# Optimization experiments

Hardware: AMD Instinct MI355X
Metric: run time of the kernel (lower is better)

## Reference

```python
import jax, jax.numpy as jnp
import numpy as np

K = 20
EPS = 1e-5   # BatchNorm eps (eval mode: running_mean=0, running_var=1)
SLOPE = 0.2


def knn_idx(x, k):
    # x: [B,F,N] -> idx [B,N,k]; top-k of negative squared distance (includes self)
    xx = jnp.sum(x * x, axis=1)                       # [B,N]
    inner = jnp.einsum('bfn,bfm->bnm', x, x)          # [B,N,N]
    neg_d = 2.0 * inner - xx[:, :, None] - xx[:, None, :]
    _, idx = jax.lax.top_k(neg_d, k)
    return idx


def gather_neighbors(x_nt, idx):
    # x_nt [B,N,F], idx [B,N,k] -> [B,N,k,F]
    return jax.vmap(lambda xt, ix: xt[ix])(x_nt, idx)


def group_layer(x_bfn, idx):
    # GroupLayer: [B,F,N] -> [B,2F,N,k] = cat(neigh - center, neigh)
    x_nt = jnp.transpose(x_bfn, (0, 2, 1))
    neigh = gather_neighbors(x_nt, idx)
    feat = jnp.concatenate([neigh - x_nt[:, :, None, :], neigh], axis=-1)
    return jnp.transpose(feat, (0, 3, 1, 2))


def eigen_graph(pts_bfn, k):
    # pts_bfn [B,3,N] -> feature [B,15,N], idx_EU [B,N,k], idx_EI [B,N,k]
    B, _, N = pts_bfn.shape
    idx_eu = knn_idx(pts_bfn, k)
    pts_nt = jnp.transpose(pts_bfn, (0, 2, 1))        # [B,N,3]
    neigh = gather_neighbors(pts_nt, idx_eu)          # [B,N,k,3]
    diff = neigh - pts_nt[:, :, None, :]
    cov = jnp.einsum('bnki,bnkj->bnij', diff, diff)   # [B,N,3,3] symmetric PSD
    eigval, eigvec = jnp.linalg.eigh(cov)             # [B,N,3], [B,N,3,3]
    feature = jnp.concatenate([pts_nt, eigval, eigvec.reshape(B, N, 9)], axis=2)
    idx_ei = knn_idx(jnp.transpose(eigval, (0, 2, 1)), k)
    return jnp.transpose(feature, (0, 2, 1)), idx_eu, idx_ei


def first_group_layer(x_bfn, idx_eu, idx_ei):
    # x_bfn [B,15,N]: [:,0:3]=xyz, [:,3:6]=eigenvalues -> [B,12,N,k]
    xyz = jnp.transpose(x_bfn[:, 0:3, :], (0, 2, 1))
    eig = jnp.transpose(x_bfn[:, 3:6, :], (0, 2, 1))
    nx = gather_neighbors(xyz, idx_eu)
    gx = jnp.concatenate([nx - xyz[:, :, None, :], nx], axis=-1)
    ne = gather_neighbors(eig, idx_ei)
    ge = jnp.concatenate([ne - eig[:, :, None, :], ne], axis=-1)
    out = jnp.concatenate([gx, ge], axis=-1)
    return jnp.transpose(out, (0, 3, 1, 2))


def graph_distance(pts_bfn, idx):
    pts_nt = jnp.transpose(pts_bfn, (0, 2, 1))
    d = gather_neighbors(pts_nt, idx) - pts_nt[:, :, None, :]
    s = jnp.sum(d * d, axis=-1)
    return jnp.sqrt(jnp.maximum(s, 1e-12))[:, None, :, :]  # [B,1,N,k]


def conv_bn_lrelu(x, w, g, b):
    # 1x1 conv (no bias) + eval-mode BN + LeakyReLU(0.2)
    if x.ndim == 4:
        y = jnp.einsum('oc,bcnk->bonk', w, x)
        g_, b_ = g[None, :, None, None], b[None, :, None, None]
    else:
        y = jnp.einsum('oc,bcn->bon', w, x)
        g_, b_ = g[None, :, None], b[None, :, None]
    y = y / jnp.sqrt(1.0 + EPS) * g_ + b_
    return jax.nn.leaky_relu(y, SLOPE)


def fps(points, n_samples):
    # furthest point sampling, start at index 0. points [B,N,3] -> [B,S] int32
    B, N, _ = points.shape
    init = jnp.zeros((B,), jnp.int32)
    dist0 = jnp.full((B, N), 1e10, points.dtype)

    def body(carry, _):
        dist, last = carry
        lastp = jnp.take_along_axis(points, last[:, None, None].astype(jnp.int32), axis=1)
        d = jnp.sum((points - lastp) ** 2, axis=-1)
        dist = jnp.minimum(dist, d)
        nxt = jnp.argmax(dist, axis=-1).astype(jnp.int32)
        return (dist, nxt), nxt

    (_, _), rest = jax.lax.scan(body, (dist0, init), None, length=n_samples - 1)
    return jnp.concatenate([init[None, :], rest], axis=0).T


def gather_op(x_bcn, idx):
    # x [B,C,N], idx [B,S] -> [B,C,S]
    return jnp.take_along_axis(x_bcn, idx[:, None, :], axis=2)


def forward(x, conv1_w, bn1_g, bn1_b, conv2_w, bn2_g, bn2_b, conv3_w, bn3_g, bn3_b,
            conv5_w, bn5_g, bn5_b, lin1_w, bn6_g, bn6_b, lin2_w, lin2_b,
            bn7_g, bn7_b, lin3_w, lin3_b):
    B, _, N1 = x.shape
    N2, N3 = N1 // 2, N1 // 4
    pts1 = jnp.transpose(x, (0, 2, 1))  # [B,N,3]

    # GSCM layer 1 (first layer)
    feat, idx_eu, idx_ei = eigen_graph(x, K)
    g = first_group_layer(feat, idx_eu, idx_ei)            # [B,12,N1,K]
    g = jnp.concatenate([g, graph_distance(x, idx_eu)], axis=1)  # [B,13,N1,K]
    x1 = conv_bn_lrelu(g, conv1_w, bn1_g, bn1_b).max(axis=-1)     # [B,64,N1]

    # downsample to N2
    id2 = fps(pts1, N2)
    pts2_bfn = gather_op(x, id2)                            # [B,3,N2]
    x1_ds = gather_op(x1, id2)                              # [B,64,N2]

    # GSCM layer 2
    _, idx_eu2, idx_ei2 = eigen_graph(pts2_bfn, K)
    g2 = jnp.concatenate([group_layer(x1_ds, idx_eu2), group_layer(x1_ds, idx_ei2)], axis=1)
    x2 = conv_bn_lrelu(g2, conv2_w, bn2_g, bn2_b).max(axis=-1)    # [B,64,N2]

    # downsample to N3
    pts2_nt = jnp.transpose(pts2_bfn, (0, 2, 1))
    id3 = fps(pts2_nt, N3)
    pts3_bfn = gather_op(pts2_bfn, id3)
    x2_ds = gather_op(x2, id3)
    x1_ds = gather_op(x1_ds, id3)

    # GSCM layer 3
    _, idx_eu3, idx_ei3 = eigen_graph(pts3_bfn, K)
    g3 = jnp.concatenate([group_layer(x2_ds, idx_eu3), group_layer(x2_ds, idx_ei3)], axis=1)
    x3 = conv_bn_lrelu(g3, conv3_w, bn3_g, bn3_b).max(axis=-1)    # [B,128,N3]

    h = jnp.concatenate([x1_ds, x2_ds, x3], axis=1)        # [B,256,N3]
    h = conv_bn_lrelu(h, conv5_w, bn5_g, bn5_b)            # [B,emb,N3]
    h = jnp.concatenate([h.max(axis=-1), h.mean(axis=-1)], axis=1)  # [B,2*emb]

    y = jnp.einsum('oi,bi->bo', lin1_w, h)
    y = jax.nn.leaky_relu(y / jnp.sqrt(1.0 + EPS) * bn6_g + bn6_b, SLOPE)
    y = jnp.einsum('oi,bi->bo', lin2_w, y) + lin2_b
    y = jax.nn.leaky_relu(y / jnp.sqrt(1.0 + EPS) * bn7_g + bn7_b, SLOPE)
    return jnp.einsum('oi,bi->bo', lin3_w, y) + lin3_b     # [B,40]


def setup_inputs() -> dict:
    key = jax.random.key(0)
    ks = jax.random.split(key, 10)
    B, N, EMB, OUT = 16, 1024, 1024, 40

    def w(k_, o, i):
        return jax.random.normal(k_, (o, i), jnp.float32) * (1.0 / np.sqrt(i))

    return {
        'x': jax.random.normal(ks[0], (B, 3, N), jnp.float32),
        'conv1_w': w(ks[1], 64, 13), 'bn1_g': jnp.ones((64,)), 'bn1_b': jnp.zeros((64,)),
        'conv2_w': w(ks[2], 64, 256), 'bn2_g': jnp.ones((64,)), 'bn2_b': jnp.zeros((64,)),
        'conv3_w': w(ks[3], 128, 256), 'bn3_g': jnp.ones((128,)), 'bn3_b': jnp.zeros((128,)),
        'conv5_w': w(ks[4], EMB, 256), 'bn5_g': jnp.ones((EMB,)), 'bn5_b': jnp.zeros((EMB,)),
        'lin1_w': w(ks[5], 512, 2 * EMB), 'bn6_g': jnp.ones((512,)), 'bn6_b': jnp.zeros((512,)),
        'lin2_w': w(ks[6], 256, 512), 'lin2_b': jnp.zeros((256,)),
        'bn7_g': jnp.ones((256,)), 'bn7_b': jnp.zeros((256,)),
        'lin3_w': w(ks[7], OUT, 256), 'lin3_b': jnp.zeros((OUT,)),
    }


def reference(x, conv1_w, bn1_g, bn1_b, conv2_w, bn2_g, bn2_b, conv3_w, bn3_g, bn3_b,
              conv5_w, bn5_g, bn5_b, lin1_w, bn6_g, bn6_b, lin2_w, lin2_b,
              bn7_g, bn7_b, lin3_w, lin3_b):
    return forward(x, conv1_w, bn1_g, bn1_b, conv2_w, bn2_g, bn2_b, conv3_w, bn3_g, bn3_b,
                   conv5_w, bn5_g, bn5_b, lin1_w, bn6_g, bn6_b, lin2_w, lin2_b,
                   bn7_g, bn7_b, lin3_w, lin3_b)
```

## Files before the change

kernel.cpp:

```cpp
#include <hip/hip_runtime.h>
#include <math.h>

#define KNB 20
constexpr float BN_INV = 0.9999950000374997f;
constexpr float SLOPE = 0.2f;

__device__ __forceinline__ float lrelu(float v){ return v >= 0.f ? v : SLOPE*v; }

__global__ __launch_bounds__(256) void prep_kernel(const float* __restrict__ x, float* __restrict__ pts,
                            const float* __restrict__ conv2w, float* __restrict__ Wc2,
                            const float* __restrict__ conv3w, float* __restrict__ Wc3){
  int i = blockIdx.x*256 + threadIdx.x;
  if (i < 16*1024){
    int b = i >> 10, n = i & 1023;
    const float* xb = x + (size_t)b*3*1024;
    float* p = pts + (size_t)i*3;
    p[0]=xb[n]; p[1]=xb[1024+n]; p[2]=xb[2048+n];
  } else if (i < 16*1024 + 64*64){
    int e = i - 16*1024;
    int o = e >> 6, c = e & 63;
    float wa=conv2w[(size_t)o*256+c], wb=conv2w[(size_t)o*256+64+c];
    float wc=conv2w[(size_t)o*256+128+c], wd=conv2w[(size_t)o*256+192+c];
    Wc2[((size_t)0*64+o)*64+c]=wa+wb; Wc2[((size_t)1*64+o)*64+c]=wc+wd; Wc2[((size_t)2*64+o)*64+c]=wa+wc;
  } else if (i < 16*1024 + 64*64 + 128*64){
    int e = i - 16*1024 - 64*64;
    int o = e >> 6, c = e & 63;
    float wa=conv3w[(size_t)o*256+c], wb=conv3w[(size_t)o*256+64+c];
    float wc=conv3w[(size_t)o*256+128+c], wd=conv3w[(size_t)o*256+192+c];
    Wc3[((size_t)0*128+o)*64+c]=wa+wb; Wc3[((size_t)1*128+o)*64+c]=wc+wd; Wc3[((size_t)2*128+o)*64+c]=wa+wc;
  }
}

template<int N, bool TOGLOBAL>
__device__ void knn_core(const float* __restrict__ pts, int* __restrict__ idx_global,
                         int* __restrict__ sOut, int chunk, int b, float4* sp){
#pragma clang fp contract(off)
  constexpr int E = N/64;
  int t = threadIdx.x;
  const float* pb = pts + (size_t)b*N*3;
  for (int e = t; e < N; e += 256){
    float x0=pb[e*3], x1=pb[e*3+1], x2=pb[e*3+2];
    sp[e] = make_float4(x0, x1, x2, (x0*x0 + x1*x1) + x2*x2);
  }
  __syncthreads();
  int wave = t >> 6, lane = t & 63;
  int row = chunk*4 + wave;
  float4 P = sp[row];
  float nd[E];
  #pragma unroll
  for (int i=0;i<E;++i){
    float4 Q = sp[lane + i*64];
    float inner = (P.x*Q.x + P.y*Q.y) + P.z*Q.z;
    nd[i] = (2.0f*inner - P.w) - Q.w;
  }
  int myout = 0;
  for (int j=0;j<KNB;++j){
    float bv = nd[0]; int bi = lane;
    #pragma unroll
    for (int i=1;i<E;++i){
      if (nd[i] > bv){ bv = nd[i]; bi = lane + i*64; }
    }
    #pragma unroll
    for (int off=1; off<64; off<<=1){
      float ov = __shfl_xor(bv, off);
      int oi = __shfl_xor(bi, off);
      if (ov > bv || (ov == bv && oi < bi)){ bv = ov; bi = oi; }
    }
    if (lane == j) myout = bi;
    if (lane == (bi & 63)){
      int slot = bi >> 6;
      #pragma unroll
      for (int i=0;i<E;++i) if (i == slot) nd[i] = -INFINITY;
    }
  }
  if (TOGLOBAL){
    if (lane < KNB) idx_global[((size_t)b*N + row)*KNB + lane] = myout;
  } else {
    if (lane < KNB) sOut[lane] = myout;
  }
}

template<int N>
__global__ __launch_bounds__(256) void knn_kernel(const float* __restrict__ pts, int* __restrict__ idx){
  __shared__ float4 sp[N];
  knn_core<N,true>(pts, idx, nullptr, blockIdx.x, blockIdx.y, sp);
}

#define DECLQ4(i) float4 Q##i = sp[(i)*256 + tid]; float D##i = 1e10f; \
  asm volatile("" : "+v"(Q##i.x), "+v"(Q##i.y), "+v"(Q##i.z));
#define UPD4(i, B) { float dx=Q##i.x-L.x; float dy=Q##i.y-L.y; float dz=Q##i.z-L.z; \
  float dd=fminf(D##i,(dx*dx+dy*dy)+dz*dz); D##i=dd; \
  unsigned long long k=((unsigned long long)__float_as_uint(dd)<<32)|(unsigned long long)(nl-(unsigned)((i)*256)); \
  if(k>B)B=k; }
#define DPPMAX(ctrl) { unsigned lo=(unsigned)bk, hi=(unsigned)(bk>>32); \
  unsigned lo2=(unsigned)__builtin_amdgcn_mov_dpp((int)lo, ctrl, 0xF, 0xF, true); \
  unsigned hi2=(unsigned)__builtin_amdgcn_mov_dpp((int)hi, ctrl, 0xF, 0xF, true); \
  unsigned long long ok=((unsigned long long)hi2<<32)|lo2; if(ok>bk)bk=ok; }
#define FPS_STEP_TAIL \
      DPPMAX(0xB1) DPPMAX(0x4E) DPPMAX(0x124) DPPMAX(0x128) \
      { unsigned long long ok=__shfl_xor(bk,16); if(ok>bk)bk=ok; } \
      { unsigned long long ok=__shfl_xor(bk,32); if(ok>bk)bk=ok; } \
      if (lane==0) rk[((s&1)<<2) | w] = bk; \
      __syncthreads(); \
      const unsigned long long* rp = rk + ((s&1)<<2); \
      unsigned long long k0=rp[0], k1=rp[1], k2=rp[2], k3=rp[3]; \
      unsigned long long km1 = k0>k1?k0:k1, km2 = k2>k3?k2:k3; \
      unsigned long long kk = km1>km2?km1:km2; \
      last = (int)(~(unsigned int)kk); \
      if (tid==0) idout[(size_t)b*M + s] = last;

template<int N, int M>
__device__ void fps_body4(const float* __restrict__ pts, int* __restrict__ idout,
                          int b, float4* sp, unsigned long long* rk){
#pragma clang fp contract(off)
  constexpr int E4 = N/256;
  int tid = threadIdx.x;
  const float* pb = pts + (size_t)b*N*3;
  for (int e=tid; e<N; e+=256){
    sp[e] = make_float4(pb[e*3], pb[e*3+1], pb[e*3+2], 0.f);
  }
  __syncthreads();
  __builtin_amdgcn_s_setprio(1);
  int lane = tid & 63, w = tid >> 6;
  unsigned int nl = ~(unsigned int)tid;
  int last = 0;
  if (tid==0) idout[(size_t)b*M] = 0;
  if constexpr (E4 == 4){
    DECLQ4(0) DECLQ4(1) DECLQ4(2) DECLQ4(3)
    for (int s=1; s<M; ++s){
      float4 L = sp[last];
      unsigned long long b0=0ULL,b1=0ULL,b2=0ULL,b3=0ULL;
      UPD4(0,b0) UPD4(1,b1) UPD4(2,b2) UPD4(3,b3)
      unsigned long long kl_ = b0>b1?b0:b1, kh_ = b2>b3?b2:b3;
      unsigned long long bk = kl_>kh_?kl_:kh_;
      FPS_STEP_TAIL
    }
  } else {
    DECLQ4(0) DECLQ4(1)
    for (int s=1; s<M; ++s){
      float4 L = sp[last];
      unsigned long long b0=0ULL,b1=0ULL;
      UPD4(0,b0) UPD4(1,b1)
      unsigned long long bk = b0>b1?b0:b1;
      FPS_STEP_TAIL
    }
  }
}

template<int N, int M>
__global__ __launch_bounds__(256, 1) void mega_knn_fps_kernel(const float* __restrict__ pts,
    int* __restrict__ knn_idx, int* __restrict__ fps_id){
  __shared__ float4 sp[N];
  __shared__ unsigned long long rk[8];
  if (blockIdx.x < 16){
    fps_body4<N,M>(pts, fps_id, blockIdx.x, sp, rk);
  } else {
    int bx = blockIdx.x - 16;
    knn_core<N,true>(pts, knn_idx, nullptr, bx % (N/4), bx / (N/4), sp);
  }
}

template<int N>
__global__ void cov_eig_kernel(const float* __restrict__ pts, const int* __restrict__ idx,
                               float* __restrict__ eigval){
  int i = blockIdx.x*blockDim.x + threadIdx.x;
  if (i >= 16*N) return;
  int b = i / N, n = i % N;
  const float* pb = pts + (size_t)b*N*3;
  const int* ix = idx + (size_t)i*KNB;
  float cx = pb[n*3], cy = pb[n*3+1], cz = pb[n*3+2];
  float c00=0,c01=0,c02=0,c11=0,c12=0,c22=0;
  for (int k=0;k<KNB;++k){
    int m = ix[k];
    float dx = pb[m*3]-cx, dy = pb[m*3+1]-cy, dz = pb[m*3+2]-cz;
    c00 += dx*dx; c01 += dx*dy; c02 += dx*dz;
    c11 += dy*dy; c12 += dy*dz; c22 += dz*dz;
  }
  double a00=c00,a01=c01,a02=c02,a11=c11,a12=c12,a22=c22;
  double p1 = a01*a01 + a02*a02 + a12*a12;
  double q = (a00+a11+a22)/3.0;
  double b00=a00-q, b11=a11-q, b22=a22-q;
  double p2 = b00*b00+b11*b11+b22*b22 + 2.0*p1;
  double e0,e1,e2;
  if (p2 <= 0.0){
    e0=e1=e2=q;
  } else {
    double p = sqrt(p2/6.0);
    double det = b00*(b11*b22 - a12*a12) - a01*(a01*b22 - a12*a02) + a02*(a01*a12 - b11*a02);
    double r = det / (2.0*p*p*p);
    r = fmin(1.0, fmax(-1.0, r));
    double phi = acos(r)/3.0;
    double big = q + 2.0*p*cos(phi);
    double sml = q + 2.0*p*cos(phi + 2.0943951023931953);
    double mid = 3.0*q - big - sml;
    e0 = sml; e1 = mid; e2 = big;
  }
  float* ev = eigval + (size_t)i*3;
  ev[0]=(float)e0; ev[1]=(float)e1; ev[2]=(float)e2;
}

__global__ __launch_bounds__(256) void knn_ei_stage1_kernel(
    const float* __restrict__ eig, const float* __restrict__ pts,
    const int* __restrict__ idx_eu,
    const float* __restrict__ w, const float* __restrict__ g, const float* __restrict__ bb,
    float* __restrict__ x1){
  constexpr int N = 1024;
  __shared__ float4 sp[N];
  __shared__ int sIei[4][KNB];
  __shared__ float feat[4][13][KNB];
  int b = blockIdx.y, chunk = blockIdx.x;
  int t = threadIdx.x, wave = t>>6, lane = t&63;
  knn_core<N,false>(eig, nullptr, &sIei[wave][0], chunk, b, sp);
  int row = chunk*4 + wave;
  size_t i = (size_t)b*N + row;
  const float* pb = pts + (size_t)b*N*3;
  if (lane < KNB){
    int ieu = idx_eu[i*KNB + lane];
    int iei = sIei[wave][lane];
    float4 ne4 = sp[iei];
    float4 ee4 = sp[row];
    float d2 = 0.f;
    #pragma unroll
    for (int f=0; f<3; ++f){
      float nx = pb[ieu*3+f], xx = pb[row*3+f];
      float dfv = nx - xx;
      feat[wave][f][lane] = dfv; feat[wave][3+f][lane] = nx;
      float ne = (f==0)? ne4.x : ((f==1)? ne4.y : ne4.z);
      float ee = (f==0)? ee4.x : ((f==1)? ee4.y : ee4.z);
      feat[wave][6+f][lane] = ne - ee; feat[wave][9+f][lane] = ne;
      d2 += dfv*dfv;
    }
    feat[wave][12][lane] = sqrtf(fmaxf(d2, 1e-12f));
  }
  __syncthreads();
  float wr[13];
  #pragma unroll
  for (int c=0;c<13;++c) wr[c] = w[lane*13+c];
  float sg = BN_INV * g[lane], sb = bb[lane];
  float mx = -INFINITY;
  for (int k=0;k<KNB;++k){
    float s = 0.f;
    #pragma unroll
    for (int c=0;c<13;++c) s = fmaf(wr[c], feat[wave][c][k], s);
    mx = fmaxf(mx, lrelu(fmaf(s, sg, sb)));
  }
  x1[i*64 + lane] = mx;
}

template<int COUT, int N>
__device__ void gm_body(const float* __restrict__ eig,
    const float* __restrict__ PQR, int Mtot,
    const int* __restrict__ idx_eu,
    const float* __restrict__ g, const float* __restrict__ bb,
    float* __restrict__ xout, int chunk, int b, float4* sp, int* sIeiW){
  int t = threadIdx.x, wave = t>>6, lane = t&63;
  knn_core<N,false>(eig, nullptr, sIeiW, chunk, b, sp);
  __syncthreads();
  int row = chunk*4 + wave;
  size_t i = (size_t)b*N + row;
  const float* P = PQR;
  const float* Q = PQR + (size_t)Mtot*COUT;
  const float* R = PQR + (size_t)2*Mtot*COUT;
  for (int o = lane; o < COUT; o += 64){
    float base = R[i*COUT + o];
    float sg = BN_INV*g[o], sb = bb[o];
    float mx = -INFINITY;
    for (int k=0;k<KNB;++k){
      int eu = idx_eu[i*KNB + k];
      int ei = sIeiW[k];
      float v = P[((size_t)b*N + eu)*COUT + o] + Q[((size_t)b*N + ei)*COUT + o] - base;
      mx = fmaxf(mx, lrelu(fmaf(v, sg, sb)));
    }
    xout[i*COUT + o] = mx;
  }
}

template<int COUT, int N>
__global__ __launch_bounds__(256) void knn_ei_gm_kernel(
    const float* __restrict__ eig, const float* __restrict__ PQR, int Mtot,
    const int* __restrict__ idx_eu, const float* __restrict__ g, const float* __restrict__ bb,
    float* __restrict__ xout){
  __shared__ float4 sp[N];
  __shared__ int sIei[4][KNB];
  int wave = threadIdx.x >> 6;
  gm_body<COUT,N>(eig, PQR, Mtot, idx_eu, g, bb, xout, blockIdx.x, blockIdx.y, sp, &sIei[wave][0]);
}

template<int COUT, int N, int M>
__global__ __launch_bounds__(256, 1) void gmfps_kernel(
    const float* __restrict__ eig, const float* __restrict__ ptsN,
    const float* __restrict__ PQR, int Mtot,
    const int* __restrict__ idx_eu, const float* __restrict__ g, const float* __restrict__ bb,
    float* __restrict__ xout, int* __restrict__ fps_id){
  __shared__ float4 sp[N];
  __shared__ int sIei[4][KNB];
  __shared__ unsigned long long rk[8];
  if (blockIdx.x < 16){
    fps_body4<N,M>(ptsN, fps_id, blockIdx.x, sp, rk);
    return;
  }
  int bx = blockIdx.x - 16;
  int wave = threadIdx.x >> 6;
  gm_body<COUT,N>(eig, PQR, Mtot, idx_eu, g, bb, xout, bx % (N/4), bx / (N/4), sp, &sIei[wave][0]);
}

__global__ __launch_bounds__(256) void gather2_kernel(const float* __restrict__ pts1, const float* __restrict__ x1,
                               const int* __restrict__ id2, float* __restrict__ pts2, float* __restrict__ x1d){
  int i = blockIdx.x*256 + threadIdx.x;
  if (i < 16*512){
    int b = i >> 9;
    int src = id2[i];
    const float* p = pts1 + ((size_t)b*1024 + src)*3;
    float* o = pts2 + (size_t)i*3;
    o[0]=p[0]; o[1]=p[1]; o[2]=p[2];
  } else {
    int e = i - 16*512;
    if (e < 16*512*64){
      int c = e & 63, r = e >> 6;
      int b = r >> 9, s = r & 511;
      int src = id2[(size_t)b*512 + s];
      x1d[e] = x1[((size_t)b*1024 + src)*64 + c];
    }
  }
}

__global__ __launch_bounds__(256) void gather3_kernel(const float* __restrict__ pts2, const float* __restrict__ x2,
                               const float* __restrict__ x1d, const int* __restrict__ id3,
                               float* __restrict__ pts3, float* __restrict__ x2d, float* __restrict__ x1dd){
  int i = blockIdx.x*256 + threadIdx.x;
  if (i < 16*256){
    int b = i >> 8;
    int src = id3[i];
    const float* p = pts2 + ((size_t)b*512 + src)*3;
    float* o = pts3 + (size_t)i*3;
    o[0]=p[0]; o[1]=p[1]; o[2]=p[2];
  } else {
    int e = i - 16*256;
    if (e < 16*256*64){
      int c = e & 63, r = e >> 6;
      int b = r >> 8, s = r & 255;
      int src = id3[(size_t)b*256 + s];
      x2d[e] = x2[((size_t)b*512 + src)*64 + c];
    } else {
      int e2 = e - 16*256*64;
      if (e2 < 16*256*64){
        int c = e2 & 63, r = e2 >> 6;
        int b = r >> 8, s = r & 255;
        int src = id3[(size_t)b*256 + s];
        x1dd[e2] = x1d[((size_t)b*512 + src)*64 + c];
      }
    }
  }
}

template<int COUT>
__global__ __launch_bounds__(256) void gemm_xw_kernel(
    const float* __restrict__ X, const float* __restrict__ Wc,
    float* __restrict__ PQR, int Mtot){
  __shared__ float sA[64][68];
  __shared__ float sW[64][68];
  int mt = blockIdx.x, ot = blockIdx.y, set = blockIdx.z;
  int t = threadIdx.x;
  for (int e=t; e<4096; e+=256){ int r=e>>6, c=e&63; sA[r][c] = X[(size_t)(mt*64+r)*64 + c]; }
  const float* Wp = Wc + ((size_t)set*COUT + ot*64)*64;
  for (int e=t; e<4096; e+=256){ int r=e>>6, c=e&63; sW[r][c] = Wp[(size_t)r*64 + c]; }
  __syncthreads();
  int tx = t & 15, ty = t >> 4;
  float acc[4][4];
  #pragma unroll
  for (int r=0;r<4;++r)
    #pragma unroll
    for (int j=0;j<4;++j) acc[r][j]=0.f;
  #pragma unroll
  for (int k4=0;k4<16;++k4){
    float4 A0 = *(const float4*)&sA[ty*4+0][k4*4];
    float4 A1 = *(const float4*)&sA[ty*4+1][k4*4];
    float4 A2 = *(const float4*)&sA[ty*4+2][k4*4];
    float4 A3 = *(const float4*)&sA[ty*4+3][k4*4];
    float4 W0 = *(const float4*)&sW[tx*4+0][k4*4];
    float4 W1 = *(const float4*)&sW[tx*4+1][k4*4];
    float4 W2 = *(const float4*)&sW[tx*4+2][k4*4];
    float4 W3 = *(const float4*)&sW[tx*4+3][k4*4];
    float4 A[4] = {A0,A1,A2,A3};
    float4 W[4] = {W0,W1,W2,W3};
    #pragma unroll
    for (int r=0;r<4;++r)
      #pragma unroll
      for (int j=0;j<4;++j){
        float s = acc[r][j];
        s = fmaf(A[r].x, W[j].x, s);
        s = fmaf(A[r].y, W[j].y, s);
        s = fmaf(A[r].z, W[j].z, s);
        s = fmaf(A[r].w, W[j].w, s);
        acc[r][j] = s;
      }
  }
  float* outp = PQR + (size_t)set*Mtot*COUT;
  #pragma unroll
  for (int r=0;r<4;++r){
    float4 v = make_float4(acc[r][0], acc[r][1], acc[r][2], acc[r][3]);
    *(float4*)&outp[(size_t)(mt*64 + ty*4 + r)*COUT + ot*64 + tx*4] = v;
  }
}

__global__ __launch_bounds__(256) void conv5_gemm_kernel(
    const float* __restrict__ x1dd, const float* __restrict__ x2d, const float* __restrict__ x3,
    const float* __restrict__ w, const float* __restrict__ g, const float* __restrict__ bb,
    float* __restrict__ pmax, float* __restrict__ psum){
  __shared__ float sA[64][68];
  __shared__ float sB[64][68];
  int otile = blockIdx.x, ntile = blockIdx.y, b = blockIdx.z;
  int t = threadIdx.x;
  int tx = t & 15, ty = t >> 4;
  float acc[4][4];
  #pragma unroll
  for (int i=0;i<4;++i)
    #pragma unroll
    for (int j=0;j<4;++j) acc[i][j] = 0.f;
  for (int kc=0; kc<4; ++kc){
    #pragma unroll 4
    for (int e = t; e < 4096; e += 256){
      int nl = e >> 6, kl = e & 63;
      int n = ntile*64 + nl;
      float v;
      if (kc == 0)      v = x1dd[((size_t)b*256 + n)*64 + kl];
      else if (kc == 1) v = x2d [((size_t)b*256 + n)*64 + kl];
      else              v = x3  [((size_t)b*256 + n)*128 + (kc-2)*64 + kl];
      sA[nl][kl] = v;
    }
    #pragma unroll 4
    for (int e = t; e < 4096; e += 256){
      int ol = e >> 6, kl = e & 63;
      sB[ol][kl] = w[((size_t)(otile*64 + ol))*256 + kc*64 + kl];
    }
    __syncthreads();
    #pragma unroll
    for (int k4=0; k4<16; ++k4){
      float4 a0 = *(const float4*)&sA[ty*4+0][k4*4];
      float4 a1 = *(const float4*)&sA[ty*4+1][k4*4];
      float4 a2 = *(const float4*)&sA[ty*4+2][k4*4];
      float4 a3 = *(const float4*)&sA[ty*4+3][k4*4];
      float4 b0 = *(const float4*)&sB[tx*4+0][k4*4];
      float4 b1 = *(const float4*)&sB[tx*4+1][k4*4];
      float4 b2 = *(const float4*)&sB[tx*4+2][k4*4];
      float4 b3 = *(const float4*)&sB[tx*4+3][k4*4];
      float4 A[4] = {a0,a1,a2,a3};
      float4 Bv[4] = {b0,b1,b2,b3};
      #pragma unroll
      for (int i=0;i<4;++i)
        #pragma unroll
        for (int j=0;j<4;++j){
          float s = acc[i][j];
          s = fmaf(A[i].x, Bv[j].x, s);
          s = fmaf(A[i].y, Bv[j].y, s);
          s = fmaf(A[i].z, Bv[j].z, s);
          s = fmaf(A[i].w, Bv[j].w, s);
          acc[i][j] = s;
        }
    }
    __syncthreads();
  }
  float sg[4], sbv[4];
  #pragma unroll
  for (int j=0;j<4;++j){
    int o = otile*64 + tx*4 + j;
    sg[j] = BN_INV*g[o]; sbv[j] = bb[o];
  }
  float mx[4], sm[4];
  #pragma unroll
  for (int j=0;j<4;++j){ mx[j]=-INFINITY; sm[j]=0.f; }
  #pragma unroll
  for (int i=0;i<4;++i)
    #pragma unroll
    for (int j=0;j<4;++j){
      float vv = lrelu(fmaf(acc[i][j], sg[j], sbv[j]));
      mx[j] = fmaxf(mx[j], vv);
      sm[j] += vv;
    }
  float* redM = &sA[0][0];
  float* redS = redM + 16*64;
  #pragma unroll
  for (int j=0;j<4;++j){
    redM[ty*64 + tx*4 + j] = mx[j];
    redS[ty*64 + tx*4 + j] = sm[j];
  }
  __syncthreads();
  if (t < 64){
    float m = -INFINITY, s = 0.f;
    #pragma unroll
    for (int r=0;r<16;++r){
      m = fmaxf(m, redM[r*64 + t]);
      s += redS[r*64 + t];
    }
    int o = otile*64 + t;
    pmax[((size_t)b*1024 + o)*4 + ntile] = m;
    psum[((size_t)b*1024 + o)*4 + ntile] = s;
  }
}

__global__ __launch_bounds__(256) void lin1_kernel(const float* __restrict__ pmax, const float* __restrict__ psum,
    const float* __restrict__ w, const float* __restrict__ g, const float* __restrict__ bb,
    float* __restrict__ y1){
  __shared__ float sh[2048];
  int b = blockIdx.y; int o = blockIdx.x*256 + threadIdx.x;
  for (int e=threadIdx.x; e<2048; e+=256){
    if (e < 1024){
      const float* pm = pmax + ((size_t)b*1024 + e)*4;
      sh[e] = fmaxf(fmaxf(pm[0],pm[1]), fmaxf(pm[2],pm[3]));
    } else {
      const float* ps = psum + ((size_t)b*1024 + (e-1024))*4;
      sh[e] = ((ps[0]+ps[1])+(ps[2]+ps[3])) * (1.0f/256.0f);
    }
  }
  __syncthreads();
  const float* wr = w + (size_t)o*2048;
  float acc=0.f;
  for (int c=0;c<2048;++c) acc = fmaf(wr[c], sh[c], acc);
  y1[(size_t)b*512+o] = lrelu(fmaf(acc, BN_INV*g[o], bb[o]));
}

__global__ __launch_bounds__(256) void lin23_kernel(const float* __restrict__ y1,
    const float* __restrict__ w2, const float* __restrict__ lb2,
    const float* __restrict__ g, const float* __restrict__ bb,
    const float* __restrict__ w3, const float* __restrict__ lb3,
    float* __restrict__ outp){
  __shared__ float sh1[512];
  __shared__ float sh2[256];
  int b = blockIdx.x; int o = threadIdx.x;
  for (int e=o; e<512; e+=256) sh1[e]=y1[(size_t)b*512+e];
  __syncthreads();
  {
    const float* wr = w2 + (size_t)o*512;
    float acc=0.f;
    for (int c=0;c<512;++c) acc = fmaf(wr[c], sh1[c], acc);
    acc += lb2[o];
    sh2[o] = lrelu(fmaf(acc, BN_INV*g[o], bb[o]));
  }
  __syncthreads();
  if (o < 40){
    const float* wr = w3 + (size_t)o*256;
    float acc=0.f;
    for (int c=0;c<256;++c) acc = fmaf(wr[c], sh2[c], acc);
    outp[(size_t)b*40+o] = acc + lb3[o];
  }
}

extern "C" void kernel_launch(void* const* d_in, const int* in_sizes, int n_in,
                              void* d_out, int out_size, void* d_ws, size_t ws_size,
                              hipStream_t stream) {
  const float* x      = (const float*)d_in[0];
  const float* conv1w = (const float*)d_in[1];
  const float* bn1g   = (const float*)d_in[2];
  const float* bn1b   = (const float*)d_in[3];
  const float* conv2w = (const float*)d_in[4];
  const float* bn2g   = (const float*)d_in[5];
  const float* bn2b   = (const float*)d_in[6];
  const float* conv3w = (const float*)d_in[7];
  const float* bn3g   = (const float*)d_in[8];
  const float* bn3b   = (const float*)d_in[9];
  const float* conv5w = (const float*)d_in[10];
  const float* bn5g   = (const float*)d_in[11];
  const float* bn5b   = (const float*)d_in[12];
  const float* lin1w  = (const float*)d_in[13];
  const float* bn6g   = (const float*)d_in[14];
  const float* bn6b   = (const float*)d_in[15];
  const float* lin2w  = (const float*)d_in[16];
  const float* lin2b  = (const float*)d_in[17];
  const float* bn7g   = (const float*)d_in[18];
  const float* bn7b   = (const float*)d_in[19];
  const float* lin3w  = (const float*)d_in[20];
  const float* lin3b  = (const float*)d_in[21];
  float* outp = (float*)d_out;

  char* ws = (char*)d_ws;
  size_t off = 0;
  auto alloc = [&](size_t bytes)->char*{
    off = (off + 255) & ~(size_t)255;
    char* p = ws + off; off += bytes; return p;
  };
  const int B=16, N1=1024, N2=512, N3=256;
  float* pts1 = (float*)alloc((size_t)B*N1*3*4);
  int*   ieu1 = (int*)alloc((size_t)B*N1*KNB*4);
  float* eig1 = (float*)alloc((size_t)B*N1*3*4);
  float* x1   = (float*)alloc((size_t)B*N1*64*4);
  int*   id2  = (int*)alloc((size_t)B*N2*4);
  float* pts2 = (float*)alloc((size_t)B*N2*3*4);
  float* x1d  = (float*)alloc((size_t)B*N2*64*4);
  int*   ieu2 = (int*)alloc((size_t)B*N2*KNB*4);
  float* eig2 = (float*)alloc((size_t)B*N2*3*4);
  float* x2   = (float*)alloc((size_t)B*N2*64*4);
  int*   id3  = (int*)alloc((size_t)B*N3*4);
  float* pts3 = (float*)alloc((size_t)B*N3*3*4);
  float* x2d  = (float*)alloc((size_t)B*N3*64*4);
  float* x1dd = (float*)alloc((size_t)B*N3*64*4);
  int*   ieu3 = (int*)alloc((size_t)B*N3*KNB*4);
  float* eig3 = (float*)alloc((size_t)B*N3*3*4);
  float* x3   = (float*)alloc((size_t)B*N3*128*4);
  float* pmax = (float*)alloc((size_t)B*1024*4*4);
  float* psum = (float*)alloc((size_t)B*1024*4*4);
  float* y1   = (float*)alloc((size_t)B*512*4);
  float* Wc2  = (float*)alloc((size_t)3*64*64*4);
  float* Wc3  = (float*)alloc((size_t)3*128*64*4);
  float* PQR2 = (float*)alloc((size_t)3*B*N2*64*4);
  float* PQR3 = (float*)alloc((size_t)3*B*N3*128*4);

  prep_kernel<<<112, 256, 0, stream>>>(x, pts1, conv2w, Wc2, conv3w, Wc3);
  mega_knn_fps_kernel<1024,512><<<16 + 4096, 256, 0, stream>>>(pts1, ieu1, id2);
  cov_eig_kernel<1024><<<(B*N1+255)/256, 256, 0, stream>>>(pts1, ieu1, eig1);
  knn_ei_stage1_kernel<<<dim3(256,16), 256, 0, stream>>>(eig1, pts1, ieu1, conv1w, bn1g, bn1b, x1);
  gather2_kernel<<<2080, 256, 0, stream>>>(pts1, x1, id2, pts2, x1d);
  knn_kernel<512><<<dim3(128,16), 256, 0, stream>>>(pts2, ieu2);
  gemm_xw_kernel<64><<<dim3(B*N2/64, 1, 3), 256, 0, stream>>>(x1d, Wc2, PQR2, B*N2);
  cov_eig_kernel<512><<<(B*N2+255)/256, 256, 0, stream>>>(pts2, ieu2, eig2);
  gmfps_kernel<64,512,256><<<16 + 2048, 256, 0, stream>>>(eig2, pts2, PQR2, B*N2, ieu2, bn2g, bn2b, x2, id3);
  gather3_kernel<<<2064, 256, 0, stream>>>(pts2, x2, x1d, id3, pts3, x2d, x1dd);
  knn_kernel<256><<<dim3(64,16), 256, 0, stream>>>(pts3, ieu3);
  cov_eig_kernel<256><<<(B*N3+255)/256, 256, 0, stream>>>(pts3, ieu3, eig3);
  gemm_xw_kernel<128><<<dim3(B*N3/64, 2, 3), 256, 0, stream>>>(x2d, Wc3, PQR3, B*N3);
  knn_ei_gm_kernel<128,256><<<dim3(64,16), 256, 0, stream>>>(eig3, PQR3, B*N3, ieu3, bn3g, bn3b, x3);
  conv5_gemm_kernel<<<dim3(16,4,16), 256, 0, stream>>>(x1dd, x2d, x3, conv5w, bn5g, bn5b, pmax, psum);
  lin1_kernel<<<dim3(2,16), 256, 0, stream>>>(pmax, psum, lin1w, bn6g, bn6b, y1);
  lin23_kernel<<<16, 256, 0, stream>>>(y1, lin2w, lin2b, bn7g, bn7b, lin3w, lin3b, outp);
}
```

Before: 660.8 us.

## Overlap first FPS with eigen-kNN stage1 and use DPP row-broadcast wave reduction

The first-level farthest-point-sampling blocks now share a launch with the eigenvalue-space kNN plus conv1 stage instead of the Euclidean kNN, and the Euclidean kNN becomes a standalone kernel again. The intent is to hide the long serial FPS chain behind a larger body of parallel work. The FPS wave reduction replaces two cross-lane shuffles with DPP row_bcast15/row_bcast31 steps and reads the result from lane 63, which should shorten the per-step latency. The cov_eig and gemm launches for level 2 are also reordered.

```diff
diff --git a/kernel.cpp b/kernel.cpp
--- a/kernel.cpp
+++ b/kernel.cpp
@@ -97,16 +97,14 @@
   unsigned hi2=(unsigned)__builtin_amdgcn_mov_dpp((int)hi, ctrl, 0xF, 0xF, true); \
   unsigned long long ok=((unsigned long long)hi2<<32)|lo2; if(ok>bk)bk=ok; }
 #define FPS_STEP_TAIL \
-      DPPMAX(0xB1) DPPMAX(0x4E) DPPMAX(0x124) DPPMAX(0x128) \
-      { unsigned long long ok=__shfl_xor(bk,16); if(ok>bk)bk=ok; } \
-      { unsigned long long ok=__shfl_xor(bk,32); if(ok>bk)bk=ok; } \
-      if (lane==0) rk[((s&1)<<2) | w] = bk; \
+      DPPMAX(0xB1) DPPMAX(0x4E) DPPMAX(0x124) DPPMAX(0x128) DPPMAX(0x142) DPPMAX(0x143) \
+      if (lane == 63) rk[((s&1)<<2) | w] = bk; \
       __syncthreads(); \
-      const unsigned long long* rp = rk + ((s&1)<<2); \
-      unsigned long long k0=rp[0], k1=rp[1], k2=rp[2], k3=rp[3]; \
-      unsigned long long km1 = k0>k1?k0:k1, km2 = k2>k3?k2:k3; \
-      unsigned long long kk = km1>km2?km1:km2; \
-      last = (int)(~(unsigned int)kk); \
+      { const unsigned long long* rp = rk + ((s&1)<<2); \
+        unsigned long long k0=rp[0], k1=rp[1], k2=rp[2], k3=rp[3]; \
+        unsigned long long km1 = k0>k1?k0:k1, km2 = k2>k3?k2:k3; \
+        unsigned long long kk = km1>km2?km1:km2; \
+        last = (int)(~(unsigned int)kk); } \
       if (tid==0) idout[(size_t)b*M + s] = last;
 
 template<int N, int M>
@@ -144,19 +142,6 @@
       unsigned long long bk = b0>b1?b0:b1;
       FPS_STEP_TAIL
     }
-  }
-}
-
-template<int N, int M>
-__global__ __launch_bounds__(256, 1) void mega_knn_fps_kernel(const float* __restrict__ pts,
-    int* __restrict__ knn_idx, int* __restrict__ fps_id){
-  __shared__ float4 sp[N];
-  __shared__ unsigned long long rk[8];
-  if (blockIdx.x < 16){
-    fps_body4<N,M>(pts, fps_id, blockIdx.x, sp, rk);
-  } else {
-    int bx = blockIdx.x - 16;
-    knn_core<N,true>(pts, knn_idx, nullptr, bx % (N/4), bx / (N/4), sp);
   }
 }
 
@@ -199,16 +184,13 @@
   ev[0]=(float)e0; ev[1]=(float)e1; ev[2]=(float)e2;
 }
 
-__global__ __launch_bounds__(256) void knn_ei_stage1_kernel(
+__device__ void stage1_body(
     const float* __restrict__ eig, const float* __restrict__ pts,
     const int* __restrict__ idx_eu,
     const float* __restrict__ w, const float* __restrict__ g, const float* __restrict__ bb,
-    float* __restrict__ x1){
+    float* __restrict__ x1, int chunk, int b,
+    float4* sp, int (*sIei)[KNB], float (*feat)[13][KNB]){
   constexpr int N = 1024;
-  __shared__ float4 sp[N];
-  __shared__ int sIei[4][KNB];
-  __shared__ float feat[4][13][KNB];
-  int b = blockIdx.y, chunk = blockIdx.x;
   int t = threadIdx.x, wave = t>>6, lane = t&63;
   knn_core<N,false>(eig, nullptr, &sIei[wave][0], chunk, b, sp);
   int row = chunk*4 + wave;
@@ -245,6 +227,23 @@
     mx = fmaxf(mx, lrelu(fmaf(s, sg, sb)));
   }
   x1[i*64 + lane] = mx;
+}
+
+__global__ __launch_bounds__(256, 1) void mega1_kernel(
+    const float* __restrict__ pts1, int* __restrict__ fps_id,
+    const float* __restrict__ eig1, const int* __restrict__ idx_eu,
+    const float* __restrict__ w, const float* __restrict__ g, const float* __restrict__ bb,
+    float* __restrict__ x1){
+  __shared__ float4 sp[1024];
+  __shared__ int sIei[4][KNB];
+  __shared__ float feat[4][13][KNB];
+  __shared__ unsigned long long rk[8];
+  if (blockIdx.x < 16){
+    fps_body4<1024,512>(pts1, fps_id, blockIdx.x, sp, rk);
+  } else {
+    int bx = blockIdx.x - 16;
+    stage1_body(eig1, pts1, idx_eu, w, g, bb, x1, bx & 255, bx >> 8, sp, sIei, feat);
+  }
 }
 
 template<int COUT, int N>
@@ -605,13 +604,13 @@
   float* PQR3 = (float*)alloc((size_t)3*B*N3*128*4);
 
   prep_kernel<<<112, 256, 0, stream>>>(x, pts1, conv2w, Wc2, conv3w, Wc3);
-  mega_knn_fps_kernel<1024,512><<<16 + 4096, 256, 0, stream>>>(pts1, ieu1, id2);
+  knn_kernel<1024><<<dim3(256,16), 256, 0, stream>>>(pts1, ieu1);
   cov_eig_kernel<1024><<<(B*N1+255)/256, 256, 0, stream>>>(pts1, ieu1, eig1);
-  knn_ei_stage1_kernel<<<dim3(256,16), 256, 0, stream>>>(eig1, pts1, ieu1, conv1w, bn1g, bn1b, x1);
+  mega1_kernel<<<16 + 4096, 256, 0, stream>>>(pts1, id2, eig1, ieu1, conv1w, bn1g, bn1b, x1);
   gather2_kernel<<<2080, 256, 0, stream>>>(pts1, x1, id2, pts2, x1d);
   knn_kernel<512><<<dim3(128,16), 256, 0, stream>>>(pts2, ieu2);
+  cov_eig_kernel<512><<<(B*N2+255)/256, 256, 0, stream>>>(pts2, ieu2, eig2);
   gemm_xw_kernel<64><<<dim3(B*N2/64, 1, 3), 256, 0, stream>>>(x1d, Wc2, PQR2, B*N2);
-  cov_eig_kernel<512><<<(B*N2+255)/256, 256, 0, stream>>>(pts2, ieu2, eig2);
   gmfps_kernel<64,512,256><<<16 + 2048, 256, 0, stream>>>(eig2, pts2, PQR2, B*N2, ieu2, bn2g, bn2b, x2, id3);
   gather3_kernel<<<2064, 256, 0, stream>>>(pts2, x2, x1d, id3, pts3, x2d, x1dd);
   knn_kernel<256><<<dim3(64,16), 256, 0, stream>>>(pts3, ieu3);
```

Result: faster. 602.1 us (-8.9%).
